# Kernel tuning notes

Hardware: AMD Instinct MI355X
Metric: run time of the kernel (lower is better)

## Reference

```python
import jax, jax.numpy as jnp
import numpy as np

VOCAB, FDIM = 100000, 256
N_NODES, N_UNIQUE, NUM_SAMPLE = 4096, 16384, 10
NEG = -9.0e15


def setup_inputs() -> dict:
    key = jax.random.key(0)
    k0, k1, k2, k3 = jax.random.split(key, 4)
    features = jax.random.normal(k0, (VOCAB, FDIM), dtype=jnp.float32)
    nodes = jax.random.randint(k1, (N_NODES,), 0, VOCAB, dtype=jnp.int64 if jax.config.jax_enable_x64 else jnp.int32)
    unique_ids = jax.random.randint(k2, (N_UNIQUE,), 0, VOCAB, dtype=nodes.dtype)
    neigh_idx = jax.random.randint(k3, (N_NODES, NUM_SAMPLE), 0, N_UNIQUE, dtype=nodes.dtype)
    return {"features": features, "nodes": nodes, "unique_ids": unique_ids, "neigh_idx": neigh_idx}


def reference(features, nodes, unique_ids, neigh_idx):
    # features: [V, F] lookup table (the `features` callable of the module)
    # nodes: [N] batch node ids; unique_ids: [M] unique sampled-neighbor ids
    # neigh_idx: [N, S] columns (into unique_ids) of each node's sampled neighbors
    N, _ = neigh_idx.shape
    M = unique_ids.shape[0]
    feature_matrix = features[nodes]        # [N, F]
    embed_matrix = features[unique_ids]     # [M, F]
    # binary adjacency mask built from (row, col) index pairs
    rows = jnp.arange(N)[:, None]           # [N, 1]
    mask = jnp.zeros((N, M), dtype=jnp.float32).at[rows, neigh_idx].set(1.0)
    scores = feature_matrix @ embed_matrix.T            # [N, M]
    scores = jnp.where(mask > 0, scores, NEG)           # masked with -9e15
    attention = jax.nn.softmax(scores, axis=1)          # softmax over dim=1
    to_feats = attention @ embed_matrix                 # [N, F]
    return to_feats
```

## Files before the change

### kernel.cpp

```cpp
#include <hip/hip_runtime.h>
#include <hip/hip_bf16.h>

#define FDIM 256
#define NSAMP 10
#define NEGF -9.0e15f


__global__ __launch_bounds__(256) void AttentionAggregator_42477226557515_kernel(
    const float* __restrict__ features,
    const int* __restrict__ nodes_w,
    const int* __restrict__ uids_w,
    const int* __restrict__ nidx_w,
    float* __restrict__ out,
    int n_nodes)
{
    const int lane = threadIdx.x & 63;
    const int n = (blockIdx.x << 2) + (threadIdx.x >> 6);
    if (n >= n_nodes) return;

    const unsigned long long oddnz = __ballot(nodes_w[2 * lane + 1] != 0);
    const bool i64 = (oddnz == 0ULL);

    const int off = lane * 4;

    const int node_id = i64 ? nodes_w[2 * n] : nodes_w[n];
    const float4 sr = *(const float4*)(features + (size_t)node_id * FDIM + off);
    const float f0 = sr.x, f1 = sr.y, f2 = sr.z, f3 = sr.w;

    int c_own = 0;
    if (lane < NSAMP) {
        const int j = n * NSAMP + lane;
        c_own = i64 ? nidx_w[2 * j] : nidx_w[j];
    }
    int u_own = 0;
    if (lane < NSAMP)
        u_own = i64 ? uids_w[2 * c_own] : uids_w[c_own];

    int cols[NSAMP], uid[NSAMP];
#pragma unroll
    for (int s = 0; s < NSAMP; ++s) {
        cols[s] = __shfl(c_own, s, 64);
        uid[s]  = __shfl(u_own, s, 64);
    }

    bool valid[NSAMP];
#pragma unroll
    for (int s = 0; s < NSAMP; ++s) {
        bool v = true;
#pragma unroll
        for (int t = 0; t < NSAMP; ++t)
            if (t < s && cols[t] == cols[s]) v = false;
        valid[s] = v;
    }

    float e[NSAMP][4];
    float ps[NSAMP];
#pragma unroll
    for (int s = 0; s < NSAMP; ++s) {
        const float4 r = *(const float4*)(features + (size_t)uid[s] * FDIM + off);
        e[s][0] = r.x; e[s][1] = r.y; e[s][2] = r.z; e[s][3] = r.w;
        ps[s] = f0 * e[s][0] + f1 * e[s][1] + f2 * e[s][2] + f3 * e[s][3];
    }

    float sc[NSAMP];
#pragma unroll
    for (int s = 0; s < NSAMP; ++s) {
        float p = ps[s];
#pragma unroll
        for (int d = 32; d > 0; d >>= 1) p += __shfl_xor(p, d, 64);
        sc[s] = valid[s] ? p : NEGF;
    }

    float m = sc[0];
#pragma unroll
    for (int s = 1; s < NSAMP; ++s) m = fmaxf(m, sc[s]);

    float w[NSAMP];
    float l = 0.0f;
#pragma unroll
    for (int s = 0; s < NSAMP; ++s) {
        w[s] = valid[s] ? __expf(sc[s] - m) : 0.0f;
        l += w[s];
    }
    const float inv = 1.0f / l;

    float o0 = 0.f, o1 = 0.f, o2 = 0.f, o3 = 0.f;
#pragma unroll
    for (int s = 0; s < NSAMP; ++s) {
        o0 += w[s] * e[s][0];
        o1 += w[s] * e[s][1];
        o2 += w[s] * e[s][2];
        o3 += w[s] * e[s][3];
    }

    float4 o;
    o.x = o0 * inv; o.y = o1 * inv; o.z = o2 * inv; o.w = o3 * inv;
    *(float4*)(out + (size_t)n * FDIM + off) = o;
}

extern "C" void kernel_launch(void* const* d_in, const int* in_sizes, int n_in,
                              void* d_out, int out_size, void* d_ws, size_t ws_size,
                              hipStream_t stream) {
    const float* features = (const float*)d_in[0];
    const int* nodes      = (const int*)d_in[1];
    const int* uids       = (const int*)d_in[2];
    const int* nidx       = (const int*)d_in[3];
    float* out            = (float*)d_out;

    const int n_nodes = out_size / FDIM;
    const int blocks  = (n_nodes + 3) / 4;

    hipLaunchKernelGGL(AttentionAggregator_42477226557515_kernel,
                       dim3(blocks), dim3(256), 0, stream,
                       features, nodes, uids, nidx, out, n_nodes);
}
```

Measured before the change: 138.2 us.

## Split each node's feature row across two wavefronts with shared-memory score combine

Each node is now handled by two wavefronts, each covering half of the feature dimension with float2 loads, and the partial dot products are combined through shared memory after a block barrier. Softmax is done lane-parallel, one sample per lane, with wave reductions, and the dedup check is computed per lane. Launch bounds request higher occupancy. The aim is more waves in flight to hide gather latency, at the cost of narrower loads, a __syncthreads and extra shuffles.

```diff
diff --git a/kernel.cpp b/kernel.cpp
--- a/kernel.cpp
+++ b/kernel.cpp
@@ -1,12 +1,12 @@
 #include <hip/hip_runtime.h>
-#include <hip/hip_bf16.h>
 
 #define FDIM 256
+#define HALF 128
 #define NSAMP 10
 #define NEGF -9.0e15f
 
 
-__global__ __launch_bounds__(256) void AttentionAggregator_42477226557515_kernel(
+__global__ __launch_bounds__(256, 8) void AttentionAggregator_42477226557515_kernel(
     const float* __restrict__ features,
     const int* __restrict__ nodes_w,
     const int* __restrict__ uids_w,
@@ -14,18 +14,22 @@
     float* __restrict__ out,
     int n_nodes)
 {
+    __shared__ float part[4][16];
+
     const int lane = threadIdx.x & 63;
-    const int n = (blockIdx.x << 2) + (threadIdx.x >> 6);
-    if (n >= n_nodes) return;
+    const int wid  = threadIdx.x >> 6;
+    const int half = wid & 1;
+    int n = (blockIdx.x << 1) + (wid >> 1);
+    const bool live = (n < n_nodes);
+    if (!live) n = 0;
 
     const unsigned long long oddnz = __ballot(nodes_w[2 * lane + 1] != 0);
     const bool i64 = (oddnz == 0ULL);
 
-    const int off = lane * 4;
+    const int off = half * HALF + (lane << 1);
 
     const int node_id = i64 ? nodes_w[2 * n] : nodes_w[n];
-    const float4 sr = *(const float4*)(features + (size_t)node_id * FDIM + off);
-    const float f0 = sr.x, f1 = sr.y, f2 = sr.z, f3 = sr.w;
+    const float2 sr = *(const float2*)(features + (size_t)node_id * FDIM + off);
 
     int c_own = 0;
     if (lane < NSAMP) {
@@ -36,66 +40,59 @@
     if (lane < NSAMP)
         u_own = i64 ? uids_w[2 * c_own] : uids_w[c_own];
 
-    int cols[NSAMP], uid[NSAMP];
+    bool vown = true;
+#pragma unroll
+    for (int t = 0; t < NSAMP; ++t) {
+        const int ct = __shfl(c_own, t, 64);
+        if (t < lane && ct == c_own) vown = false;
+    }
+
+    float2 e[NSAMP];
 #pragma unroll
     for (int s = 0; s < NSAMP; ++s) {
-        cols[s] = __shfl(c_own, s, 64);
-        uid[s]  = __shfl(u_own, s, 64);
+        const int u = __shfl(u_own, s, 64);
+        e[s] = *(const float2*)(features + (size_t)u * FDIM + off);
     }
 
-    bool valid[NSAMP];
+    float part_own = 0.0f;
 #pragma unroll
     for (int s = 0; s < NSAMP; ++s) {
-        bool v = true;
+        float p = sr.x * e[s].x + sr.y * e[s].y;
 #pragma unroll
-        for (int t = 0; t < NSAMP; ++t)
-            if (t < s && cols[t] == cols[s]) v = false;
-        valid[s] = v;
+        for (int d = 32; d > 0; d >>= 1) p += __shfl_xor(p, d, 64);
+        if (lane == s) part_own = p;
     }
 
-    float e[NSAMP][4];
-    float ps[NSAMP];
+    if (lane < NSAMP) part[wid][lane] = part_own;
+    __syncthreads();
+    const int partner = wid ^ 1;
+    float sc_own = NEGF;
+    if (lane < NSAMP && vown)
+        sc_own = part[wid][lane] + part[partner][lane];
+
+    float m = sc_own;
+#pragma unroll
+    for (int d = 32; d > 0; d >>= 1) m = fmaxf(m, __shfl_xor(m, d, 64));
+    float w_own = (lane < NSAMP && vown) ? __expf(sc_own - m) : 0.0f;
+    float l = w_own;
+#pragma unroll
+    for (int d = 32; d > 0; d >>= 1) l += __shfl_xor(l, d, 64);
+    const float inv = 1.0f / l;
+
+    float a0 = 0.0f, a1 = 0.0f;
 #pragma unroll
     for (int s = 0; s < NSAMP; ++s) {
-        const float4 r = *(const float4*)(features + (size_t)uid[s] * FDIM + off);
-        e[s][0] = r.x; e[s][1] = r.y; e[s][2] = r.z; e[s][3] = r.w;
-        ps[s] = f0 * e[s][0] + f1 * e[s][1] + f2 * e[s][2] + f3 * e[s][3];
+        const float ws = __shfl(w_own, s, 64);
+        a0 += ws * e[s].x;
+        a1 += ws * e[s].y;
     }
 
-    float sc[NSAMP];
-#pragma unroll
-    for (int s = 0; s < NSAMP; ++s) {
-        float p = ps[s];
-#pragma unroll
-        for (int d = 32; d > 0; d >>= 1) p += __shfl_xor(p, d, 64);
-        sc[s] = valid[s] ? p : NEGF;
+    if (live) {
+        float2 o;
+        o.x = a0 * inv;
+        o.y = a1 * inv;
+        *(float2*)(out + (size_t)n * FDIM + off) = o;
     }
-
-    float m = sc[0];
-#pragma unroll
-    for (int s = 1; s < NSAMP; ++s) m = fmaxf(m, sc[s]);
-
-    float w[NSAMP];
-    float l = 0.0f;
-#pragma unroll
-    for (int s = 0; s < NSAMP; ++s) {
-        w[s] = valid[s] ? __expf(sc[s] - m) : 0.0f;
-        l += w[s];
-    }
-    const float inv = 1.0f / l;
-
-    float o0 = 0.f, o1 = 0.f, o2 = 0.f, o3 = 0.f;
-#pragma unroll
-    for (int s = 0; s < NSAMP; ++s) {
-        o0 += w[s] * e[s][0];
-        o1 += w[s] * e[s][1];
-        o2 += w[s] * e[s][2];
-        o3 += w[s] * e[s][3];
-    }
-
-    float4 o;
-    o.x = o0 * inv; o.y = o1 * inv; o.z = o2 * inv; o.w = o3 * inv;
-    *(float4*)(out + (size_t)n * FDIM + off) = o;
 }
 
 extern "C" void kernel_launch(void* const* d_in, const int* in_sizes, int n_in,
@@ -108,7 +105,7 @@
     float* out            = (float*)d_out;
 
     const int n_nodes = out_size / FDIM;
-    const int blocks  = (n_nodes + 3) / 4;
+    const int blocks  = (n_nodes + 1) / 2;
 
     hipLaunchKernelGGL(AttentionAggregator_42477226557515_kernel,
                        dim3(blocks), dim3(256), 0, stream,
```

Result: slower. 143.0 us (+3.5%).
